# Performance work log

Measured on AMD Instinct MI355X. Metric: run time of the kernel, lower is better.

Reference implementation:

```python
import jax, jax.numpy as jnp
import numpy as np

N_ATOMS = 500000
N_BONDS = 1000000
NODE = 128
EDGE = 16
OUT = 128
DEGREES = (1, 2, 3, 4)
COUNTS = (50000, 150000, 200000, 100000)  # sums to N_ATOMS
EPS = 1e-5


def setup_inputs() -> dict:
    key = jax.random.key(0)
    ks = jax.random.split(key, 16)
    atom_repr = jax.random.normal(ks[0], (N_ATOMS, NODE), dtype=jnp.float32)
    bond_repr = jax.random.normal(ks[1], (N_BONDS, EDGE), dtype=jnp.float32)
    # first column of each degree group's atom index list is the node's own id;
    # the union of first columns is a permutation of 0..N_ATOMS-1 (every node in exactly one group)
    perm = jax.random.permutation(ks[2], N_ATOMS)
    inp = {"atom_repr": atom_repr, "bond_repr": bond_repr}
    off = 0
    for i, (d, n) in enumerate(zip(DEGREES, COUNTS)):
        own = perm[off:off + n][:, None]
        nbrs = jax.random.randint(ks[3 + 2 * i], (n, d), 0, N_ATOMS)
        inp[f"atom_idx_{d}"] = jnp.concatenate([own, nbrs], axis=1).astype(jnp.int32)
        inp[f"bond_idx_{d}"] = jax.random.randint(ks[4 + 2 * i], (n, d), 0, N_BONDS).astype(jnp.int32)
        off += n
    # parameters (torch Linear weights stored here as [in, out])
    s = 1.0 / np.sqrt(NODE)
    inp["W_self"] = jax.random.uniform(ks[11], (NODE, OUT), jnp.float32, -s, s)
    sd = 1.0 / np.sqrt(NODE + EDGE)
    inp["W1"] = jax.random.uniform(ks[12], (NODE + EDGE, OUT), jnp.float32, -sd, sd)
    inp["W2"] = jax.random.uniform(ks[13], (NODE + EDGE, OUT), jnp.float32, -sd, sd)
    inp["W3"] = jax.random.uniform(ks[14], (NODE + EDGE, OUT), jnp.float32, -sd, sd)
    inp["W4"] = jax.random.uniform(ks[15], (NODE + EDGE, OUT), jnp.float32, -sd, sd)
    inp["bias"] = jnp.zeros((1, OUT), dtype=jnp.float32)
    return inp


def reference(atom_repr, bond_repr, W_self, W1, W2, W3, W4, bias,
              atom_idx_1, atom_idx_2, atom_idx_3, atom_idx_4,
              bond_idx_1, bond_idx_2, bond_idx_3, bond_idx_4):
    Ws = (W1, W2, W3, W4)
    aidxs = (atom_idx_1, atom_idx_2, atom_idx_3, atom_idx_4)
    bidxs = (bond_idx_1, bond_idx_2, bond_idx_3, bond_idx_4)
    n = atom_repr.shape[0]
    neighbor_repr = jnp.zeros((n, OUT), dtype=atom_repr.dtype)
    for W, aidx, bidx in zip(Ws, aidxs, bidxs):
        a_sum = atom_repr[aidx].sum(axis=1)      # [n_d, NODE] (includes self, per original)
        b_sum = bond_repr[bidx].sum(axis=1)      # [n_d, EDGE]
        act = jnp.concatenate([a_sum, b_sum], axis=1) @ W  # [n_d, OUT]
        # scatter back to node order (equivalent to concat + argsort by atoms[0])
        neighbor_repr = neighbor_repr.at[aidx[:, 0]].set(act)
    self_repr = atom_repr @ W_self
    x = self_repr + neighbor_repr + bias
    # BatchNorm1d(affine=False), training mode: biased batch stats
    mean = x.mean(axis=0)
    var = x.var(axis=0)
    x = (x - mean) * jax.lax.rsqrt(var + EPS)
    return jax.nn.relu(x)
```

## Files before the change

### kernel.cpp

```cpp
#include <hip/hip_runtime.h>
#include <hip/hip_bf16.h>
#include <math.h>

#define N_ATOMS 500000
#define EPS 1e-5f
#define LDA 296

#define NB1 55
#define NB2 249
#define NB3 443
#define NB4 277
#define NBLK 1024

#define SEG_ELEMS 36864

typedef __attribute__((ext_vector_type(8))) short short8;
typedef __attribute__((ext_vector_type(4))) float floatx4;

__device__ __forceinline__ unsigned short f2bf(float f) {
    unsigned int x = __float_as_uint(f);
    x += 0x7FFF + ((x >> 16) & 1);
    return (unsigned short)(x >> 16);
}

__device__ __forceinline__ float4 add4(float4 a, float4 b) {
    return make_float4(a.x + b.x, a.y + b.y, a.z + b.z, a.w + b.w);
}

__device__ __forceinline__ void st_bf4(unsigned short* p, float4 v) {
    ushort4 u;
    u.x = f2bf(v.x); u.y = f2bf(v.y); u.z = f2bf(v.z); u.w = f2bf(v.w);
    *reinterpret_cast<ushort4*>(p) = u;
}

__global__ __launch_bounds__(256) void gdc_pack(
    const float* __restrict__ W1, const float* __restrict__ W2,
    const float* __restrict__ W3, const float* __restrict__ W4,
    const float* __restrict__ Wself, unsigned short* __restrict__ packed)
{
    const int t = blockIdx.x * 256 + threadIdx.x;
    if (t >= 4 * 9 * 8 * 64) return;
    const int d    = t / 4608;
    const int r    = t % 4608;
    const int ks   = r / 512;
    const int nt   = (r % 512) / 64;
    const int lane = r % 64;
    const float* Wd = (d == 0) ? W1 : (d == 1) ? W2 : (d == 2) ? W3 : W4;
    const int col = nt * 16 + (lane & 15);
    short8 v;
    #pragma unroll
    for (int j = 0; j < 8; ++j) {
        const int k = ks * 32 + ((lane >> 4) << 3) + j;
        float w = 0.f;
        if (k < 144)      w = Wd[k * 128 + col];
        else if (k < 272) w = Wself[(k - 144) * 128 + col];
        v[j] = (short)f2bf(w);
    }
    *reinterpret_cast<short8*>(packed + (size_t)d * SEG_ELEMS
                               + ((size_t)(ks * 8 + nt) * 64 + lane) * 8) = v;
}

template <int DEG>
__device__ __forceinline__ void block_loop(
    const float* __restrict__ atom, const float* __restrict__ bond,
    const int* __restrict__ aidx, const int* __restrict__ bidx,
    const unsigned short* __restrict__ pw,
    float* __restrict__ out,
    unsigned short* __restrict__ A, int* __restrict__ own_lds,
    int n, int lb, int nb, int tid, int lane, int wv)
{
    const int m    = tid >> 4;
    const int q16  = tid & 15;
    const int ccol = lane & 15;
    const int crow = lane >> 4;
    const int nbase = wv * 16;

    short8 bfr[9];
    #pragma unroll
    for (int ks = 0; ks < 9; ++ks)
        bfr[ks] = ((const short8*)pw)[(ks * 8 + wv) * 64 + lane];

    float psum = 0.f, psq = 0.f;
    const int tiles = (n + 31) >> 5;

    for (int t = lb; t < tiles; t += nb) {
        const int i0 = t << 5;
        const int i = i0 + m;

        if (i < n) {
            const int* ar = aidx + (size_t)i * (DEG + 1);
            const int own = ar[0];
            if (q16 == 0) own_lds[m] = own;
            const float4* s = (const float4*)(atom + (size_t)own * 128 + q16 * 8);
            float4 a0 = s[0], a1 = s[1];
            unsigned short* rowp = A + m * LDA;
            st_bf4(rowp + 144 + q16 * 8 + 0, a0);
            st_bf4(rowp + 144 + q16 * 8 + 4, a1);
            #pragma unroll
            for (int j = 1; j <= DEG; ++j) {
                const float4* p = (const float4*)(atom + (size_t)ar[j] * 128 + q16 * 8);
                a0 = add4(a0, p[0]); a1 = add4(a1, p[1]);
            }
            st_bf4(rowp + q16 * 8 + 0, a0);
            st_bf4(rowp + q16 * 8 + 4, a1);
            if (q16 < 8) {
                const int* br = bidx + (size_t)i * DEG;
                float bx = 0.f, by = 0.f;
                #pragma unroll
                for (int j = 0; j < DEG; ++j) {
                    const float2 bb = *(const float2*)(bond + (size_t)br[j] * 16 + q16 * 2);
                    bx += bb.x; by += bb.y;
                }
                unsigned short* pb = rowp + 128 + q16 * 2;
                pb[0] = f2bf(bx); pb[1] = f2bf(by);
            }
        }
        __syncthreads();

        floatx4 acc0 = (floatx4){0.f, 0.f, 0.f, 0.f};
        floatx4 acc1 = (floatx4){0.f, 0.f, 0.f, 0.f};
        #pragma unroll
        for (int ks = 0; ks < 9; ++ks) {
            const short8 af0 = *(const short8*)&A[ccol * LDA + ks * 32 + (crow << 3)];
            const short8 af1 = *(const short8*)&A[(16 + ccol) * LDA + ks * 32 + (crow << 3)];
            acc0 = __builtin_amdgcn_mfma_f32_16x16x32_bf16(af0, bfr[ks], acc0, 0, 0, 0);
            acc1 = __builtin_amdgcn_mfma_f32_16x16x32_bf16(af1, bfr[ks], acc1, 0, 0, 0);
        }

        const int4 o0 = *reinterpret_cast<const int4*>(&own_lds[crow * 4]);
        const int4 o1 = *reinterpret_cast<const int4*>(&own_lds[16 + crow * 4]);
        const int owns0[4] = {o0.x, o0.y, o0.z, o0.w};
        const int owns1[4] = {o1.x, o1.y, o1.z, o1.w};
        #pragma unroll
        for (int rr = 0; rr < 4; ++rr) {
            const int row = crow * 4 + rr;
            if (i0 + row < n) {
                const float v = acc0[rr];
                out[(size_t)owns0[rr] * 128 + nbase + ccol] = v;
                psum += v; psq += v * v;
            }
            if (i0 + 16 + row < n) {
                const float v = acc1[rr];
                out[(size_t)owns1[rr] * 128 + nbase + ccol] = v;
                psum += v; psq += v * v;
            }
        }
        __syncthreads();
    }

    float* redS = reinterpret_cast<float*>(A);
    float* redQ = redS + 128;
    {
        float s = psum, q = psq;
        s += __shfl_xor(s, 16, 64); s += __shfl_xor(s, 32, 64);
        q += __shfl_xor(q, 16, 64); q += __shfl_xor(q, 32, 64);
        if (lane < 16) {
            redS[nbase + lane] = s;
            redQ[nbase + lane] = q;
        }
    }
}

__global__ __launch_bounds__(512, 4) void gdc_mfma(
    const float* __restrict__ atom, const float* __restrict__ bond,
    const int* __restrict__ a1, const int* __restrict__ b1,
    const int* __restrict__ a2, const int* __restrict__ b2,
    const int* __restrict__ a3, const int* __restrict__ b3,
    const int* __restrict__ a4, const int* __restrict__ b4,
    const unsigned short* __restrict__ packedW,
    float* __restrict__ out,
    float* __restrict__ sumPart, float* __restrict__ sqPart)
{
    __shared__ __align__(16) unsigned short A[32 * LDA];
    __shared__ __align__(16) int own_lds[32];

    const int tid  = threadIdx.x;
    const int wv   = tid >> 6;
    const int lane = tid & 63;
    const int blk  = blockIdx.x;

    int n, lb, nb, deg;
    const int* aidx; const int* bidx;
    if (blk < NB1)                 { deg = 1; n =  50000; lb = blk;                 nb = NB1; aidx = a1; bidx = b1; }
    else if (blk < NB1+NB2)        { deg = 2; n = 150000; lb = blk-NB1;             nb = NB2; aidx = a2; bidx = b2; }
    else if (blk < NB1+NB2+NB3)    { deg = 3; n = 200000; lb = blk-(NB1+NB2);       nb = NB3; aidx = a3; bidx = b3; }
    else                           { deg = 4; n = 100000; lb = blk-(NB1+NB2+NB3);   nb = NB4; aidx = a4; bidx = b4; }

    const unsigned short* pw = packedW + (size_t)(deg - 1) * SEG_ELEMS;

    {
        const int mm = tid >> 4, qq = tid & 15;
        if (qq >= 8) {
            ushort2 z; z.x = 0; z.y = 0;
            *reinterpret_cast<ushort2*>(&A[mm * LDA + 272 + (qq - 8) * 2]) = z;
        }
    }
    __syncthreads();

    switch (deg) {
    case 1:  block_loop<1>(atom, bond, aidx, bidx, pw, out, A, own_lds, n, lb, nb, tid, lane, wv); break;
    case 2:  block_loop<2>(atom, bond, aidx, bidx, pw, out, A, own_lds, n, lb, nb, tid, lane, wv); break;
    case 3:  block_loop<3>(atom, bond, aidx, bidx, pw, out, A, own_lds, n, lb, nb, tid, lane, wv); break;
    default: block_loop<4>(atom, bond, aidx, bidx, pw, out, A, own_lds, n, lb, nb, tid, lane, wv); break;
    }

    __syncthreads();
    const float* redS = reinterpret_cast<const float*>(A);
    if (tid < 128)      sumPart[(size_t)blk * 128 + tid] = redS[tid];
    else if (tid < 256) sqPart[(size_t)blk * 128 + (tid - 128)] = redS[tid];
}

__global__ void gdc_stats(const float* __restrict__ sumPart,
                          const float* __restrict__ sqPart,
                          float* __restrict__ mv)
{
    const int c = blockIdx.x;
    const int j = threadIdx.x;
    __shared__ float rs[256], rq[256];
    float s = 0.f, q = 0.f;
    for (int b = j; b < NBLK; b += 256) {
        s += sumPart[(size_t)b * 128 + c];
        q += sqPart[(size_t)b * 128 + c];
    }
    rs[j] = s; rq[j] = q;
    __syncthreads();
    for (int off = 128; off > 0; off >>= 1) {
        if (j < off) { rs[j] += rs[j + off]; rq[j] += rq[j + off]; }
        __syncthreads();
    }
    if (j == 0) {
        const float mean = rs[0] / (float)N_ATOMS;
        const float var  = rq[0] / (float)N_ATOMS - mean * mean;
        mv[c]       = mean;
        mv[128 + c] = rsqrtf(var + EPS);
    }
}

__global__ __launch_bounds__(256) void gdc_norm(float* __restrict__ out,
                                                const float* __restrict__ mv)
{
    const size_t total4 = (size_t)N_ATOMS * 128 / 4;
    size_t idx = (size_t)blockIdx.x * 256 + threadIdx.x;
    const int c = (int)((idx * 4) & 127);
    const float4 m  = *(const float4*)(mv + c);
    const float4 iv = *(const float4*)(mv + 128 + c);
    const size_t stride = (size_t)gridDim.x * 256;
    for (; idx < total4; idx += stride) {
        float4 v = ((float4*)out)[idx];
        v.x = fmaxf(0.f, (v.x - m.x) * iv.x);
        v.y = fmaxf(0.f, (v.y - m.y) * iv.y);
        v.z = fmaxf(0.f, (v.z - m.z) * iv.z);
        v.w = fmaxf(0.f, (v.w - m.w) * iv.w);
        ((float4*)out)[idx] = v;
    }
}

extern "C" void kernel_launch(void* const* d_in, const int* in_sizes, int n_in,
                              void* d_out, int out_size, void* d_ws, size_t ws_size,
                              hipStream_t stream) {
    const float* atom  = (const float*)d_in[0];
    const float* bond  = (const float*)d_in[1];
    const int*   a1    = (const int*)d_in[2];
    const int*   b1    = (const int*)d_in[3];
    const int*   a2    = (const int*)d_in[4];
    const int*   b2    = (const int*)d_in[5];
    const int*   a3    = (const int*)d_in[6];
    const int*   b3    = (const int*)d_in[7];
    const int*   a4    = (const int*)d_in[8];
    const int*   b4    = (const int*)d_in[9];
    const float* Wself = (const float*)d_in[10];
    const float* W1    = (const float*)d_in[11];
    const float* W2    = (const float*)d_in[12];
    const float* W3    = (const float*)d_in[13];
    const float* W4    = (const float*)d_in[14];
    float* out = (float*)d_out;

    unsigned short* packedW = (unsigned short*)d_ws;
    float* sumPart = (float*)((char*)d_ws + 4 * SEG_ELEMS * sizeof(unsigned short));
    float* sqPart  = sumPart + (size_t)NBLK * 128;
    float* mv      = sqPart + (size_t)NBLK * 128;

    hipLaunchKernelGGL(gdc_pack, dim3((4*9*8*64 + 255)/256), dim3(256), 0, stream,
                       W1, W2, W3, W4, Wself, packedW);
    hipLaunchKernelGGL(gdc_mfma, dim3(NBLK), dim3(512), 0, stream,
                       atom, bond, a1, b1, a2, b2, a3, b3, a4, b4,
                       packedW, out, sumPart, sqPart);
    hipLaunchKernelGGL(gdc_stats, dim3(128), dim3(256), 0, stream,
                       sumPart, sqPart, mv);
    hipLaunchKernelGGL(gdc_norm, dim3(2048), dim3(256), 0, stream, out, mv);
}
```

Measured before the change: 351.9 us.

## Double-buffer LDS tiles and prefetch next tile's gathers during MFMA

The per-tile loop now keeps two LDS buffers and uses register prefetching. The next tile's atom and bond gathers are issued after the barrier, so they overlap the current tile's MFMA work and scatter stores, and neighbour indices are fetched two tiles ahead. This drops one __syncthreads per iteration. In exchange, LDS use doubles to about 38KB per block and register pressure rises, which may limit occupancy at launch_bounds(512,4). Tail rows are clamped to n-1 rather than skipped.

```diff
diff --git a/kernel.cpp b/kernel.cpp
--- a/kernel.cpp
+++ b/kernel.cpp
@@ -82,53 +82,102 @@
 
     float psum = 0.f, psq = 0.f;
     const int tiles = (n + 31) >> 5;
-
-    for (int t = lb; t < tiles; t += nb) {
-        const int i0 = t << 5;
-        const int i = i0 + m;
-
-        if (i < n) {
-            const int* ar = aidx + (size_t)i * (DEG + 1);
-            const int own = ar[0];
-            if (q16 == 0) own_lds[m] = own;
-            const float4* s = (const float4*)(atom + (size_t)own * 128 + q16 * 8);
-            float4 a0 = s[0], a1 = s[1];
-            unsigned short* rowp = A + m * LDA;
-            st_bf4(rowp + 144 + q16 * 8 + 0, a0);
-            st_bf4(rowp + 144 + q16 * 8 + 4, a1);
+    const int nmax  = n - 1;
+
+    float4 self0, self1, sum0, sum1;
+    float bx, by;
+    int own_r;
+    int ni[DEG + 1];
+    {
+        const int i = min((lb << 5) + m, nmax);
+        const int* ar = aidx + (size_t)i * (DEG + 1);
+        #pragma unroll
+        for (int j = 0; j <= DEG; ++j) ni[j] = ar[j];
+        own_r = ni[0];
+        const float4* s = (const float4*)(atom + (size_t)own_r * 128 + q16 * 8);
+        self0 = s[0]; self1 = s[1];
+        sum0 = self0; sum1 = self1;
+        #pragma unroll
+        for (int j = 1; j <= DEG; ++j) {
+            const float4* pp = (const float4*)(atom + (size_t)ni[j] * 128 + q16 * 8);
+            sum0 = add4(sum0, pp[0]); sum1 = add4(sum1, pp[1]);
+        }
+        bx = 0.f; by = 0.f;
+        if (q16 < 8) {
+            const int* br = bidx + (size_t)i * DEG;
+            #pragma unroll
+            for (int j = 0; j < DEG; ++j) {
+                const float2 bb = *(const float2*)(bond + (size_t)br[j] * 16 + q16 * 2);
+                bx += bb.x; by += bb.y;
+            }
+        }
+        const int t1 = min(lb + nb, tiles - 1);
+        const int i1 = min((t1 << 5) + m, nmax);
+        const int* ar1 = aidx + (size_t)i1 * (DEG + 1);
+        #pragma unroll
+        for (int j = 0; j <= DEG; ++j) ni[j] = ar1[j];
+    }
+
+    int k = 0;
+    for (int t = lb; t < tiles; t += nb, ++k) {
+        unsigned short* Ab = A + (k & 1) * (32 * LDA);
+        int* ob = own_lds + (k & 1) * 32;
+
+        {
+            unsigned short* rowp = Ab + m * LDA;
+            st_bf4(rowp + 144 + q16 * 8 + 0, self0);
+            st_bf4(rowp + 144 + q16 * 8 + 4, self1);
+            st_bf4(rowp + q16 * 8 + 0, sum0);
+            st_bf4(rowp + q16 * 8 + 4, sum1);
+            if (q16 < 8) {
+                rowp[128 + q16 * 2]     = f2bf(bx);
+                rowp[128 + q16 * 2 + 1] = f2bf(by);
+            }
+            if (q16 == 0) ob[m] = own_r;
+        }
+        __syncthreads();
+
+        if (t + nb < tiles) {
+            const int i = min(((t + nb) << 5) + m, nmax);
+            own_r = ni[0];
+            const float4* s = (const float4*)(atom + (size_t)own_r * 128 + q16 * 8);
+            self0 = s[0]; self1 = s[1];
+            float4 ns0 = self0, ns1 = self1;
             #pragma unroll
             for (int j = 1; j <= DEG; ++j) {
-                const float4* p = (const float4*)(atom + (size_t)ar[j] * 128 + q16 * 8);
-                a0 = add4(a0, p[0]); a1 = add4(a1, p[1]);
-            }
-            st_bf4(rowp + q16 * 8 + 0, a0);
-            st_bf4(rowp + q16 * 8 + 4, a1);
+                const float4* pp = (const float4*)(atom + (size_t)ni[j] * 128 + q16 * 8);
+                ns0 = add4(ns0, pp[0]); ns1 = add4(ns1, pp[1]);
+            }
+            sum0 = ns0; sum1 = ns1;
+            bx = 0.f; by = 0.f;
             if (q16 < 8) {
                 const int* br = bidx + (size_t)i * DEG;
-                float bx = 0.f, by = 0.f;
                 #pragma unroll
                 for (int j = 0; j < DEG; ++j) {
                     const float2 bb = *(const float2*)(bond + (size_t)br[j] * 16 + q16 * 2);
                     bx += bb.x; by += bb.y;
                 }
-                unsigned short* pb = rowp + 128 + q16 * 2;
-                pb[0] = f2bf(bx); pb[1] = f2bf(by);
-            }
-        }
-        __syncthreads();
+            }
+            const int t2 = min(t + 2 * nb, tiles - 1);
+            const int i2 = min((t2 << 5) + m, nmax);
+            const int* ar2 = aidx + (size_t)i2 * (DEG + 1);
+            #pragma unroll
+            for (int j = 0; j <= DEG; ++j) ni[j] = ar2[j];
+        }
 
         floatx4 acc0 = (floatx4){0.f, 0.f, 0.f, 0.f};
         floatx4 acc1 = (floatx4){0.f, 0.f, 0.f, 0.f};
         #pragma unroll
         for (int ks = 0; ks < 9; ++ks) {
-            const short8 af0 = *(const short8*)&A[ccol * LDA + ks * 32 + (crow << 3)];
-            const short8 af1 = *(const short8*)&A[(16 + ccol) * LDA + ks * 32 + (crow << 3)];
+            const short8 af0 = *(const short8*)&Ab[ccol * LDA + ks * 32 + (crow << 3)];
+            const short8 af1 = *(const short8*)&Ab[(16 + ccol) * LDA + ks * 32 + (crow << 3)];
             acc0 = __builtin_amdgcn_mfma_f32_16x16x32_bf16(af0, bfr[ks], acc0, 0, 0, 0);
             acc1 = __builtin_amdgcn_mfma_f32_16x16x32_bf16(af1, bfr[ks], acc1, 0, 0, 0);
         }
 
-        const int4 o0 = *reinterpret_cast<const int4*>(&own_lds[crow * 4]);
-        const int4 o1 = *reinterpret_cast<const int4*>(&own_lds[16 + crow * 4]);
+        const int i0 = t << 5;
+        const int4 o0 = *reinterpret_cast<const int4*>(&ob[crow * 4]);
+        const int4 o1 = *reinterpret_cast<const int4*>(&ob[16 + crow * 4]);
         const int owns0[4] = {o0.x, o0.y, o0.z, o0.w};
         const int owns1[4] = {o1.x, o1.y, o1.z, o1.w};
         #pragma unroll
@@ -145,8 +194,9 @@
                 psum += v; psq += v * v;
             }
         }
-        __syncthreads();
-    }
+    }
+
+    __syncthreads();
 
     float* redS = reinterpret_cast<float*>(A);
     float* redQ = redS + 128;
@@ -171,8 +221,8 @@
     float* __restrict__ out,
     float* __restrict__ sumPart, float* __restrict__ sqPart)
 {
-    __shared__ __align__(16) unsigned short A[32 * LDA];
-    __shared__ __align__(16) int own_lds[32];
+    __shared__ __align__(16) unsigned short A[2 * 32 * LDA];
+    __shared__ __align__(16) int own_lds[2 * 32];
 
     const int tid  = threadIdx.x;
     const int wv   = tid >> 6;
@@ -193,6 +243,7 @@
         if (qq >= 8) {
             ushort2 z; z.x = 0; z.y = 0;
             *reinterpret_cast<ushort2*>(&A[mm * LDA + 272 + (qq - 8) * 2]) = z;
+            *reinterpret_cast<ushort2*>(&A[32 * LDA + mm * LDA + 272 + (qq - 8) * 2]) = z;
         }
     }
     __syncthreads();
```

Result: faster. 340.0 us (-3.4%).
